# Kernel tuning notes

Hardware: AMD Instinct MI355X
Metric: run time of the kernel (lower is better)

The kernel has to match this reference:

```python
import jax, jax.numpy as jnp
import numpy as np

K, D = 8, 32            # num_heads, out_dim
NA, NP_, DIN = 50000, 100000, 128
SLOPE = 0.2


def _leaky(x):
    return jnp.where(x >= 0, x, SLOPE * x)


def _micro(fs, fd, attn, src, dst, n_dst):
    """GAT-style micro conv for one relation.
    fs: (N_src, K, D) projected src feats; fd: (N_dst, K, D); attn: (K, 2D).
    Returns relu'd aggregation (N_dst, K, D)."""
    al, ar = attn[:, :D], attn[:, D:]
    el = (fs * al).sum(-1)                     # (N_src, K)
    er = (fd * ar).sum(-1)                     # (N_dst, K)
    e = _leaky(el[src] + er[dst])              # (E, K)
    m = jax.ops.segment_max(e, dst, num_segments=n_dst)
    a = jnp.exp(e - m[dst])
    s = jax.ops.segment_sum(a, dst, num_segments=n_dst)
    a = a / s[dst]                             # edge softmax over incoming edges
    msg = fs[src] * a[..., None]               # (E, K, D)
    out = jax.ops.segment_sum(msg, dst, num_segments=n_dst)
    return jax.nn.relu(out)


def setup_inputs() -> dict:
    key = jax.random.key(0)
    ks = jax.random.split(key, 24)
    w = lambda k, sh: (jax.random.normal(k, sh, jnp.float32) * 0.05)
    inp = {
        'feat_author': jax.random.normal(ks[0], (NA, DIN), jnp.float32),
        'feat_paper': jax.random.normal(ks[1], (NP_, DIN), jnp.float32),
        'W_micro_author': w(ks[2], (DIN, K * D)),
        'W_micro_paper': w(ks[3], (DIN, K * D)),
        'attn_micro_author': w(ks[4], (K, 2 * D)),
        'attn_micro_paper': w(ks[5], (K, 2 * D)),
        'W_macro_node_author': w(ks[6], (DIN, K * D)),
        'W_macro_node_paper': w(ks[7], (DIN, K * D)),
        'W_rel_writes': w(ks[8], (K * D, K * D)),
        'W_rel_written_by': w(ks[9], (K * D, K * D)),
        'W_rel_cites': w(ks[10], (K * D, K * D)),
        'attn_macro': w(ks[11], (K, 2 * D)),
        'W_res_author': w(ks[12], (DIN, K * D)),
        'b_res_author': jnp.zeros((K * D,), jnp.float32),
        'W_res_paper': w(ks[13], (DIN, K * D)),
        'b_res_paper': jnp.zeros((K * D,), jnp.float32),
        'res_w_author': jax.random.uniform(ks[14], (1,), jnp.float32),
        'res_w_paper': jax.random.uniform(ks[15], (1,), jnp.float32),
        'writes_src': jax.random.randint(ks[16], (500000,), 0, NA, jnp.int32),
        'writes_dst': jax.random.randint(ks[17], (500000,), 0, NP_, jnp.int32),
        'wb_src': jax.random.randint(ks[18], (500000,), 0, NP_, jnp.int32),
        'wb_dst': jax.random.randint(ks[19], (500000,), 0, NA, jnp.int32),
        'cites_src': jax.random.randint(ks[20], (1000000,), 0, NP_, jnp.int32),
        'cites_dst': jax.random.randint(ks[21], (1000000,), 0, NP_, jnp.int32),
    }
    return inp


def reference(feat_author, feat_paper, W_micro_author, W_micro_paper,
              attn_micro_author, attn_micro_paper, W_macro_node_author,
              W_macro_node_paper, W_rel_writes, W_rel_written_by, W_rel_cites,
              attn_macro, W_res_author, b_res_author, W_res_paper, b_res_paper,
              res_w_author, res_w_paper, writes_src, writes_dst, wb_src, wb_dst,
              cites_src, cites_dst):
    # ---- micro-level (per-relation GAT) ----
    fa = (feat_author @ W_micro_author).reshape(NA, K, D)
    fp = (feat_paper @ W_micro_paper).reshape(NP_, K, D)
    r_writes = _micro(fa, fp, attn_micro_author, writes_src, writes_dst, NP_)   # (NP,K,D)
    r_wb = _micro(fp, fa, attn_micro_paper, wb_src, wb_dst, NA)                 # (NA,K,D)
    r_cites = _micro(fp, fp, attn_micro_paper, cites_src, cites_dst, NP_)       # (NP,K,D)

    # ---- macro-level (cross-relation attention) ----
    rf_writes = (r_writes.reshape(NP_, K * D) @ W_rel_writes).reshape(NP_, K, D)
    rf_wb = (r_wb.reshape(NA, K * D) @ W_rel_written_by).reshape(NA, K, D)
    rf_cites = (r_cites.reshape(NP_, K * D) @ W_rel_cites).reshape(NP_, K, D)

    # author: single incoming relation -> passthrough
    out_a = rf_wb.reshape(NA, K * D)

    # paper: two relations -> stacked attention over relation axis
    node_p = (feat_paper @ W_macro_node_paper).reshape(NP_, K, D)
    stacked = jnp.stack([rf_writes, rf_cites], axis=0)            # (2, NP, K, D)
    cat = jnp.concatenate(
        [jnp.broadcast_to(node_p, stacked.shape), stacked], axis=-1)  # (2, NP, K, 2D)
    scores = _leaky((attn_macro * cat).sum(-1, keepdims=True))    # (2, NP, K, 1)
    wgt = jax.nn.softmax(scores, axis=0)
    out_p = (wgt * stacked).sum(0).reshape(NP_, K * D)

    # ---- residual ----
    aa = jax.nn.sigmoid(res_w_author)
    out_a = aa * out_a + (1 - aa) * (feat_author @ W_res_author + b_res_author)
    ap = jax.nn.sigmoid(res_w_paper)
    out_p = ap * out_p + (1 - ap) * (feat_paper @ W_res_paper + b_res_paper)
    return out_a, out_p
```

## Files before the change

kernel.cpp:

```cpp
#include <hip/hip_runtime.h>
#include <hip/hip_bf16.h>
#include <cstddef>
#include <cstdint>

#define NAU 50000
#define NPA 100000
#define KH 8
#define DH 32
#define KD 256
#define DIN 128
#define SLOPE 0.2f

typedef __attribute__((ext_vector_type(8))) short short8;
typedef __attribute__((ext_vector_type(4))) float f32x4;

__device__ __forceinline__ float leakyf(float x) { return x >= 0.f ? x : SLOPE * x; }

__device__ __forceinline__ ushort f2b(float f) {
  __hip_bfloat16 h = __float2bfloat16(f);
  return *reinterpret_cast<ushort*>(&h);
}
__device__ __forceinline__ float b2f(ushort u) {
  __hip_bfloat16 h;
  *reinterpret_cast<ushort*>(&h) = u;
  return __bfloat162float(h);
}


__device__ __forceinline__ short8 ldfrag(const ushort (*P)[40], int row, int kq) {
  const ushort* p0 = &P[row][kq * 4];
  ushort4 a = *reinterpret_cast<const ushort4*>(p0);
  ushort4 b = *reinterpret_cast<const ushort4*>(p0 + 16);
  short8 f;
  f[0] = (short)a.x; f[1] = (short)a.y; f[2] = (short)a.z; f[3] = (short)a.w;
  f[4] = (short)b.x; f[5] = (short)b.y; f[6] = (short)b.z; f[7] = (short)b.w;
  return f;
}

template<int NP, int EPI>
__global__ __launch_bounds__(256) void k_mfma(
    const float* __restrict__ A0, int K0, const ushort* __restrict__ B0h, const ushort* __restrict__ B0l,
    const float* __restrict__ A1, int K1, const ushort* __restrict__ B1h, const ushort* __restrict__ B1l,
    const float* __restrict__ A2, int K2, const ushort* __restrict__ B2h, const ushort* __restrict__ B2l,
    int M,
    const float* __restrict__ bres, const float* __restrict__ resw,
    const float* __restrict__ wwp, const float* __restrict__ wcp,
    float* __restrict__ outp)
{
  __shared__ ushort As[2][64][40];
  __shared__ ushort Bs[2][64][40];
  const int tid = threadIdx.x;
  const int row0 = blockIdx.x * 64, col0 = blockIdx.y * 64;
  const int wid = tid >> 6, lane = tid & 63;
  const int wr = wid >> 1, wc = wid & 1;
  const int kq = lane >> 4, rr = lane & 15;
  const int sr = tid >> 2;
  const int sc = (tid & 3) << 3;

  f32x4 acc[NP][2][2] = {};

  const float*  Aps[3] = {A0, A1, A2};
  const ushort* Bhs[3] = {B0h, B1h, B2h};
  const ushort* Bls[3] = {B0l, B1l, B2l};
  const int     Kds[3] = {K0, K1, K2};

#pragma unroll
  for (int p = 0; p < NP; ++p) {
    const float*  A  = Aps[p];
    const ushort* Bh = Bhs[p];
    const ushort* Bl = Bls[p];
    const int     Kd = Kds[p];
    for (int k0 = 0; k0 < Kd; k0 += 32) {
      __syncthreads();
      {
        int gr = row0 + sr;
        float4 v0, v1;
        if (gr < M) {
          const float* ap = A + (size_t)gr * Kd + k0 + sc;
          v0 = *reinterpret_cast<const float4*>(ap);
          v1 = *reinterpret_cast<const float4*>(ap + 4);
        } else {
          v0 = make_float4(0.f, 0.f, 0.f, 0.f); v1 = v0;
        }
        float vb[8] = {v0.x, v0.y, v0.z, v0.w, v1.x, v1.y, v1.z, v1.w};
        union Pack { ushort u[8]; int4 v; } ph, pl;
#pragma unroll
        for (int i = 0; i < 8; ++i) {
          ushort h = f2b(vb[i]);
          ph.u[i] = h;
          pl.u[i] = f2b(vb[i] - b2f(h));
        }
        *reinterpret_cast<int4*>(&As[0][sr][sc]) = ph.v;
        *reinterpret_cast<int4*>(&As[1][sr][sc]) = pl.v;
      }
      {
        const size_t bo = (size_t)(col0 + sr) * Kd + k0 + sc;
        *reinterpret_cast<int4*>(&Bs[0][sr][sc]) = *reinterpret_cast<const int4*>(Bh + bo);
        *reinterpret_cast<int4*>(&Bs[1][sr][sc]) = *reinterpret_cast<const int4*>(Bl + bo);
      }
      __syncthreads();

      short8 ah[2], al[2], bh[2], bl[2];
#pragma unroll
      for (int fm = 0; fm < 2; ++fm) {
        int row = wr * 32 + fm * 16 + rr;
        ah[fm] = ldfrag(As[0], row, kq);
        al[fm] = ldfrag(As[1], row, kq);
      }
#pragma unroll
      for (int fn = 0; fn < 2; ++fn) {
        int nrow = wc * 32 + fn * 16 + rr;
        bh[fn] = ldfrag(Bs[0], nrow, kq);
        bl[fn] = ldfrag(Bs[1], nrow, kq);
      }
#pragma unroll
      for (int fm = 0; fm < 2; ++fm)
#pragma unroll
        for (int fn = 0; fn < 2; ++fn) {
          f32x4 c = acc[p][fm][fn];
          c = __builtin_amdgcn_mfma_f32_16x16x32_bf16(ah[fm], bh[fn], c, 0, 0, 0);
          c = __builtin_amdgcn_mfma_f32_16x16x32_bf16(ah[fm], bl[fn], c, 0, 0, 0);
          c = __builtin_amdgcn_mfma_f32_16x16x32_bf16(al[fm], bh[fn], c, 0, 0, 0);
          acc[p][fm][fn] = c;
        }
    }
  }

  float g = 0.f;
  if constexpr (EPI >= 1) g = 1.f / (1.f + __expf(-resw[0]));
#pragma unroll
  for (int fm = 0; fm < 2; ++fm)
#pragma unroll
    for (int fn = 0; fn < 2; ++fn) {
      int cc = col0 + wc * 32 + fn * 16 + rr;
#pragma unroll
      for (int i = 0; i < 4; ++i) {
        int r = row0 + wr * 32 + fm * 16 + kq * 4 + i;
        if (r < M) {
          if constexpr (EPI == 0) {
            outp[(size_t)r * KD + cc] = acc[0][fm][fn][i];
          } else if constexpr (EPI == 1) {
            float o = g * acc[0][fm][fn][i] + (1.f - g) * (acc[1][fm][fn][i] + bres[cc]);
            outp[(size_t)r * KD + cc] = o;
          } else {
            int head = cc >> 5;
            float wwv = wwp[(size_t)r * KH + head];
            float wcv = wcp[(size_t)r * KH + head];
            float o = g * (wwv * acc[0][fm][fn][i] + wcv * acc[1][fm][fn][i])
                    + (1.f - g) * (acc[2][fm][fn][i] + bres[cc]);
            outp[(size_t)r * KD + cc] = o;
          }
        }
      }
    }
}

__global__ void k_prepB(const float* __restrict__ W, int Kd,
                        ushort* __restrict__ Bh, ushort* __restrict__ Bl) {
  int idx = blockIdx.x * 256 + threadIdx.x;
  if (idx >= Kd * 256) return;
  int n = idx / Kd, k = idx - n * Kd;
  float v = W[(size_t)k * 256 + n];
  ushort h = f2b(v);
  Bh[idx] = h;
  Bl[idx] = f2b(v - b2f(h));
}

__global__ void k_node_dots(
    const float* __restrict__ f, int N,
    const float* __restrict__ a0, float* __restrict__ o0,
    const float* __restrict__ a1, float* __restrict__ o1,
    const float* __restrict__ a2, float* __restrict__ o2)
{
  int idx = blockIdx.x * blockDim.x + threadIdx.x;
  if (idx >= N * KH) return;
  int n = idx >> 3, k = idx & 7;
  const float* fr = f + (size_t)n * KD + k * DH;
  float d0 = 0.f, d1 = 0.f, d2 = 0.f;
#pragma unroll
  for (int i = 0; i < DH; i += 4) {
    float4 fv = *reinterpret_cast<const float4*>(fr + i);
    if (a0) {
      float4 v = *reinterpret_cast<const float4*>(a0 + k * 64 + i);
      d0 += fv.x * v.x + fv.y * v.y + fv.z * v.z + fv.w * v.w;
    }
    if (a1) {
      float4 v = *reinterpret_cast<const float4*>(a1 + k * 64 + i);
      d1 += fv.x * v.x + fv.y * v.y + fv.z * v.z + fv.w * v.w;
    }
    if (a2) {
      float4 v = *reinterpret_cast<const float4*>(a2 + k * 64 + i);
      d2 += fv.x * v.x + fv.y * v.y + fv.z * v.z + fv.w * v.w;
    }
  }
  if (o0) o0[idx] = d0;
  if (o1) o1[idx] = d1;
  if (o2) o2[idx] = d2;
}

__global__ void k_hist(const int* __restrict__ dst, int E, int* __restrict__ cnt) {
  int e = blockIdx.x * 256 + threadIdx.x;
  if (e < E) atomicAdd(&cnt[dst[e]], 1);
}

__global__ void k_scan1(const int* __restrict__ cnt, int n,
                        int* __restrict__ off, int* __restrict__ bsum) {
  __shared__ int sm[256];
  int t = threadIdx.x;
  int i = blockIdx.x * 256 + t;
  int v = (i < n) ? cnt[i] : 0;
  sm[t] = v; __syncthreads();
  for (int o = 1; o < 256; o <<= 1) {
    int x = (t >= o) ? sm[t - o] : 0;
    __syncthreads();
    sm[t] += x;
    __syncthreads();
  }
  if (i < n) off[i] = sm[t] - v;
  if (t == 255) bsum[blockIdx.x] = sm[255];
}

__global__ void k_scan2(int* __restrict__ bsum, int nb) {
  __shared__ int sm[512];
  int t = threadIdx.x;
  int v = (t < nb) ? bsum[t] : 0;
  sm[t] = v; __syncthreads();
  for (int o = 1; o < 512; o <<= 1) {
    int x = (t >= o) ? sm[t - o] : 0;
    __syncthreads();
    sm[t] += x;
    __syncthreads();
  }
  if (t < nb) bsum[t] = sm[t] - v;
}

__global__ void k_scan3(int* __restrict__ off, int n, const int* __restrict__ bsum) {
  int i = blockIdx.x * 256 + threadIdx.x;
  if (i < n) off[i] += bsum[blockIdx.x];
}

__global__ void k_scatter(const int* __restrict__ dst, int E,
                          const int* __restrict__ off, int* __restrict__ cur,
                          int* __restrict__ eidx) {
  int e = blockIdx.x * 256 + threadIdx.x;
  if (e >= E) return;
  int d = dst[e];
  int p = atomicAdd(&cur[d], 1);
  eidx[off[d] + p] = e;
}

__global__ __launch_bounds__(256) void k_agg_dst(
    const int* __restrict__ eidx, const int* __restrict__ off_,
    const int* __restrict__ cnt_, const int* __restrict__ src,
    const float* __restrict__ el, const float* __restrict__ er,
    const float* __restrict__ fs, float* __restrict__ outp)
{
  __shared__ int ssi[256];
  int d = blockIdx.x;
  int t = threadIdx.x;
  int k = t >> 5;
  int c = cnt_[d];
  float acc = 0.f;
  float s = 0.f;
  if (c > 0) {
    int base = off_[d];
    float erk = er[(size_t)d * KH + k];
    for (int j0 = 0; j0 < c; j0 += 256) {
      int m = min(256, c - j0);
      __syncthreads();
      if (t < m) ssi[t] = src[eidx[base + j0 + t]];
      __syncthreads();
      for (int j = 0; j < m; ++j) {
        int si = ssi[j];
        float a = __expf(leakyf(el[(size_t)si * KH + k] + erk));
        s += a;
        acc = fmaf(fs[(size_t)si * KD + t], a, acc);
      }
    }
    acc = fmaxf(acc / s, 0.f);
  }
  outp[(size_t)d * KD + t] = acc;
}

__global__ void k_weff(
    const float* __restrict__ Wmnp, const float* __restrict__ Wrw,
    const float* __restrict__ Wrc, const float* __restrict__ attn,
    float* __restrict__ enp, float* __restrict__ ew, float* __restrict__ ec)
{
  int idx = blockIdx.x * blockDim.x + threadIdx.x;
  if (idx < DIN * KH) {
    int c = idx >> 3, k = idx & 7;
    float sum = 0.f;
    for (int d = 0; d < DH; ++d) sum += Wmnp[(size_t)c * KD + k * DH + d] * attn[k * 64 + d];
    enp[idx] = sum;
  } else if (idx < DIN * KH + KD * KH) {
    int j = idx - DIN * KH;
    int c = j >> 3, k = j & 7;
    float sum = 0.f;
    for (int d = 0; d < DH; ++d) sum += Wrw[(size_t)c * KD + k * DH + d] * attn[k * 64 + 32 + d];
    ew[j] = sum;
  } else if (idx < DIN * KH + 2 * KD * KH) {
    int j = idx - DIN * KH - KD * KH;
    int c = j >> 3, k = j & 7;
    float sum = 0.f;
    for (int d = 0; d < DH; ++d) sum += Wrc[(size_t)c * KD + k * DH + d] * attn[k * 64 + 32 + d];
    ec[j] = sum;
  }
}

template<bool RELU>
__global__ __launch_bounds__(256) void k_skinny(
    const float* __restrict__ A, int M, int Kdim,
    const float* __restrict__ W, float* __restrict__ outp)
{
  __shared__ float Ws[KD * KH];
  int tid = threadIdx.x;
  for (int i = tid; i < Kdim * KH; i += 256) Ws[i] = W[i];
  __syncthreads();
  int r = blockIdx.x * 32 + (tid >> 3);
  int k = tid & 7;
  if (r >= M) return;
  const float* Ar = A + (size_t)r * Kdim;
  float acc = 0.f;
  for (int c = 0; c < Kdim; c += 4) {
    float4 av = *reinterpret_cast<const float4*>(Ar + c);
    if (RELU) {
      av.x = fmaxf(av.x, 0.f); av.y = fmaxf(av.y, 0.f);
      av.z = fmaxf(av.z, 0.f); av.w = fmaxf(av.w, 0.f);
    }
    acc += av.x * Ws[(c + 0) * KH + k] + av.y * Ws[(c + 1) * KH + k]
         + av.z * Ws[(c + 2) * KH + k] + av.w * Ws[(c + 3) * KH + k];
  }
  outp[(size_t)r * KH + k] = acc;
}

__global__ void k_weights(
    const float* __restrict__ npdot, const float* __restrict__ scw,
    const float* __restrict__ scc, float* __restrict__ ww,
    float* __restrict__ wc, int N8)
{
  int idx = blockIdx.x * blockDim.x + threadIdx.x;
  if (idx >= N8) return;
  float nd = npdot[idx];
  float lw = leakyf(nd + scw[idx]);
  float lc = leakyf(nd + scc[idx]);
  float m = fmaxf(lw, lc);
  float e1 = __expf(lw - m), e2 = __expf(lc - m);
  float inv = 1.f / (e1 + e2);
  ww[idx] = e1 * inv;
  wc[idx] = e2 * inv;
}

static inline void run_relation(hipStream_t stream,
                                const int* src, const int* dst, int E, int n_dst,
                                int* cnt, int* cur, int* off, int* bsum, int* eidx,
                                const float* el, const float* er,
                                const float* fs, float* outp) {
  hipMemsetAsync(cnt, 0, (size_t)n_dst * sizeof(int), stream);
  hipMemsetAsync(cur, 0, (size_t)n_dst * sizeof(int), stream);
  int nb = (n_dst + 255) / 256;
  k_hist<<<(E + 255) / 256, 256, 0, stream>>>(dst, E, cnt);
  k_scan1<<<nb, 256, 0, stream>>>(cnt, n_dst, off, bsum);
  k_scan2<<<1, 512, 0, stream>>>(bsum, nb);
  k_scan3<<<nb, 256, 0, stream>>>(off, n_dst, bsum);
  k_scatter<<<(E + 255) / 256, 256, 0, stream>>>(dst, E, off, cur, eidx);
  k_agg_dst<<<n_dst, 256, 0, stream>>>(eidx, off, cnt, src, el, er, fs, outp);
}

extern "C" void kernel_launch(void* const* d_in, const int* in_sizes, int n_in,
                              void* d_out, int out_size, void* d_ws, size_t ws_size,
                              hipStream_t stream)
{
  const float* feat_a  = (const float*)d_in[0];
  const float* feat_p  = (const float*)d_in[1];
  const float* W_mic_a = (const float*)d_in[2];
  const float* W_mic_p = (const float*)d_in[3];
  const float* attn_a  = (const float*)d_in[4];
  const float* attn_p  = (const float*)d_in[5];
  const float* W_mnp   = (const float*)d_in[7];
  const float* W_rw    = (const float*)d_in[8];
  const float* W_rwb   = (const float*)d_in[9];
  const float* W_rc    = (const float*)d_in[10];
  const float* attn_m  = (const float*)d_in[11];
  const float* W_res_a = (const float*)d_in[12];
  const float* b_res_a = (const float*)d_in[13];
  const float* W_res_p = (const float*)d_in[14];
  const float* b_res_p = (const float*)d_in[15];
  const float* rw_a    = (const float*)d_in[16];
  const float* rw_p    = (const float*)d_in[17];
  const int* w_src  = (const int*)d_in[18];
  const int* w_dst  = (const int*)d_in[19];
  const int* wbsrc  = (const int*)d_in[20];
  const int* wbdst  = (const int*)d_in[21];
  const int* c_src  = (const int*)d_in[22];
  const int* c_dst  = (const int*)d_in[23];
  const int Ew = in_sizes[18], Ewb = in_sizes[20], Ec = in_sizes[22];

  float* ws = (float*)d_ws;
  const size_t SA = (size_t)NAU * KD;
  const size_t SP = (size_t)NPA * KD;
  float* fa    = ws;
  float* fp    = fa + SA;
  float* r_w   = fp + SP;
  float* r_wb  = r_w + SP;
  float* r_c   = r_wb + SA;
  float* elA   = r_c + SP;
  float* erA   = elA + (size_t)NAU * KH;
  float* elP   = erA + (size_t)NAU * KH;
  float* erPa  = elP + (size_t)NPA * KH;
  float* erPp  = erPa + (size_t)NPA * KH;
  float* npdot = erPp + (size_t)NPA * KH;
  float* scw   = npdot + (size_t)NPA * KH;
  float* scc   = scw + (size_t)NPA * KH;
  float* wwb   = scc + (size_t)NPA * KH;
  float* wcb   = wwb + (size_t)NPA * KH;
  float* effnp = wcb + (size_t)NPA * KH;
  float* effw  = effnp + DIN * KH;
  float* effc  = effw + KD * KH;
  ushort* bt = (ushort*)(effc + KD * KH);
  ushort* BTmicA_h = bt;                  bt += 256 * DIN;
  ushort* BTmicA_l = bt;                  bt += 256 * DIN;
  ushort* BTmicP_h = bt;                  bt += 256 * DIN;
  ushort* BTmicP_l = bt;                  bt += 256 * DIN;
  ushort* BTrwb_h  = bt;                  bt += 256 * KD;
  ushort* BTrwb_l  = bt;                  bt += 256 * KD;
  ushort* BTrw_h   = bt;                  bt += 256 * KD;
  ushort* BTrw_l   = bt;                  bt += 256 * KD;
  ushort* BTrc_h   = bt;                  bt += 256 * KD;
  ushort* BTrc_l   = bt;                  bt += 256 * KD;
  ushort* BTresA_h = bt;                  bt += 256 * DIN;
  ushort* BTresA_l = bt;                  bt += 256 * DIN;
  ushort* BTresP_h = bt;                  bt += 256 * DIN;
  ushort* BTresP_l = bt;                  bt += 256 * DIN;
  int*   cnt   = (int*)bt;
  int*   cur   = cnt + NPA;
  int*   off   = cur + NPA;
  int*   bsum  = off + NPA;
  int*   eidx  = bsum + 512;

  float* out_a = (float*)d_out;
  float* out_p = (float*)d_out + SA;

  k_prepB<<<DIN, 256, 0, stream>>>(W_mic_a, DIN, BTmicA_h, BTmicA_l);
  k_prepB<<<DIN, 256, 0, stream>>>(W_mic_p, DIN, BTmicP_h, BTmicP_l);
  k_prepB<<<KD,  256, 0, stream>>>(W_rwb,  KD,  BTrwb_h,  BTrwb_l);
  k_prepB<<<KD,  256, 0, stream>>>(W_rw,   KD,  BTrw_h,   BTrw_l);
  k_prepB<<<KD,  256, 0, stream>>>(W_rc,   KD,  BTrc_h,   BTrc_l);
  k_prepB<<<DIN, 256, 0, stream>>>(W_res_a, DIN, BTresA_h, BTresA_l);
  k_prepB<<<DIN, 256, 0, stream>>>(W_res_p, DIN, BTresP_h, BTresP_l);

  {
    dim3 g((NAU + 63) / 64, 4);
    k_mfma<1, 0><<<g, 256, 0, stream>>>(
        feat_a, DIN, BTmicA_h, BTmicA_l,
        nullptr, 0, nullptr, nullptr, nullptr, 0, nullptr, nullptr,
        NAU, nullptr, nullptr, nullptr, nullptr, fa);
  }
  {
    dim3 g((NPA + 63) / 64, 4);
    k_mfma<1, 0><<<g, 256, 0, stream>>>(
        feat_p, DIN, BTmicP_h, BTmicP_l,
        nullptr, 0, nullptr, nullptr, nullptr, 0, nullptr, nullptr,
        NPA, nullptr, nullptr, nullptr, nullptr, fp);
  }

  k_node_dots<<<(NAU * KH + 255) / 256, 256, 0, stream>>>(
      fa, NAU, attn_a, elA, attn_p + 32, erA, nullptr, nullptr);
  k_node_dots<<<(NPA * KH + 255) / 256, 256, 0, stream>>>(
      fp, NPA, attn_p, elP, attn_a + 32, erPa, attn_p + 32, erPp);

  run_relation(stream, w_src, w_dst, Ew, NPA, cnt, cur, off, bsum, eidx,
               elA, erPa, fa, r_w);
  run_relation(stream, wbsrc, wbdst, Ewb, NAU, cnt, cur, off, bsum, eidx,
               elP, erA, fp, r_wb);
  run_relation(stream, c_src, c_dst, Ec, NPA, cnt, cur, off, bsum, eidx,
               elP, erPp, fp, r_c);

  {
    dim3 g((NAU + 63) / 64, 4);
    k_mfma<2, 1><<<g, 256, 0, stream>>>(
        r_wb, KD, BTrwb_h, BTrwb_l,
        feat_a, DIN, BTresA_h, BTresA_l,
        nullptr, 0, nullptr, nullptr,
        NAU, b_res_a, rw_a, nullptr, nullptr, out_a);
  }

  k_weff<<<20, 256, 0, stream>>>(W_mnp, W_rw, W_rc, attn_m, effnp, effw, effc);
  k_skinny<false><<<(NPA + 31) / 32, 256, 0, stream>>>(feat_p, NPA, DIN, effnp, npdot);
  k_skinny<true ><<<(NPA + 31) / 32, 256, 0, stream>>>(r_w, NPA, KD, effw, scw);
  k_skinny<true ><<<(NPA + 31) / 32, 256, 0, stream>>>(r_c, NPA, KD, effc, scc);
  k_weights<<<(NPA * KH + 255) / 256, 256, 0, stream>>>(npdot, scw, scc, wwb, wcb, NPA * KH);

  {
    dim3 g((NPA + 63) / 64, 4);
    k_mfma<3, 2><<<g, 256, 0, stream>>>(
        r_w, KD, BTrw_h, BTrw_l,
        r_c, KD, BTrc_h, BTrc_l,
        feat_p, DIN, BTresP_h, BTresP_l,
        NPA, b_res_p, rw_p, wwb, wcb, out_p);
  }
}
```

Before: 1.532 ms.

## Fuse macro score dots into aggregation, swizzle GEMM LDS, remap workgroups, unroll gather

The macro-attention score dot products (r_w·effw, r_c·effc) are now computed in the epilogue of the per-destination aggregation kernel through wave shuffles. This removes two separate skinny passes that re-read the 100k×256 relation outputs. The MFMA GEMM changes its LDS layout to a single 64-wide XOR-swizzled tile holding hi and lo halves, so each fragment is one 16-byte load. It also replaces the bf16 conversion with truncating bit masks and launches a 1D grid with an XCD-aware workgroup remap. The aggregation inner loop is unrolled by four to keep more gathers in flight. Truncating instead of rounding for the hi part changes the split-bf16 precision slightly.

```diff
diff --git a/kernel.cpp b/kernel.cpp
--- a/kernel.cpp
+++ b/kernel.cpp
@@ -27,14 +27,8 @@
 }
 
 
-__device__ __forceinline__ short8 ldfrag(const ushort (*P)[40], int row, int kq) {
-  const ushort* p0 = &P[row][kq * 4];
-  ushort4 a = *reinterpret_cast<const ushort4*>(p0);
-  ushort4 b = *reinterpret_cast<const ushort4*>(p0 + 16);
-  short8 f;
-  f[0] = (short)a.x; f[1] = (short)a.y; f[2] = (short)a.z; f[3] = (short)a.w;
-  f[4] = (short)b.x; f[5] = (short)b.y; f[6] = (short)b.z; f[7] = (short)b.w;
-  return f;
+__device__ __forceinline__ short8 ldfrag8(const ushort (*P)[64], int row, int slot) {
+  return *reinterpret_cast<const short8*>(&P[row][((slot ^ (row & 7)) << 3)]);
 }
 
 template<int NP, int EPI>
@@ -47,15 +41,22 @@
     const float* __restrict__ wwp, const float* __restrict__ wcp,
     float* __restrict__ outp)
 {
-  __shared__ ushort As[2][64][40];
-  __shared__ ushort Bs[2][64][40];
+  __shared__ ushort As[64][64];
+  __shared__ ushort Bs[64][64];
   const int tid = threadIdx.x;
-  const int row0 = blockIdx.x * 64, col0 = blockIdx.y * 64;
+
+  const int nwg = gridDim.x;
+  int orig = blockIdx.x;
+  int q = nwg >> 3, r8 = nwg & 7, xc = orig & 7, jj = orig >> 3;
+  int wg = (xc < r8 ? xc * (q + 1) : r8 * (q + 1) + (xc - r8) * q) + jj;
+  const int row0 = (wg >> 2) * 64, col0 = (wg & 3) * 64;
+
   const int wid = tid >> 6, lane = tid & 63;
   const int wr = wid >> 1, wc = wid & 1;
   const int kq = lane >> 4, rr = lane & 15;
   const int sr = tid >> 2;
-  const int sc = (tid & 3) << 3;
+  const int sq = tid & 3;
+  const int swz = sr & 7;
 
   f32x4 acc[NP][2][2] = {};
 
@@ -74,29 +75,36 @@
       __syncthreads();
       {
         int gr = row0 + sr;
-        float4 v0, v1;
+        float4 v0 = make_float4(0.f, 0.f, 0.f, 0.f), v1 = v0;
         if (gr < M) {
-          const float* ap = A + (size_t)gr * Kd + k0 + sc;
+          const float* ap = A + (size_t)gr * Kd + k0 + sq * 8;
           v0 = *reinterpret_cast<const float4*>(ap);
           v1 = *reinterpret_cast<const float4*>(ap + 4);
-        } else {
-          v0 = make_float4(0.f, 0.f, 0.f, 0.f); v1 = v0;
         }
-        float vb[8] = {v0.x, v0.y, v0.z, v0.w, v1.x, v1.y, v1.z, v1.w};
-        union Pack { ushort u[8]; int4 v; } ph, pl;
-#pragma unroll
-        for (int i = 0; i < 8; ++i) {
-          ushort h = f2b(vb[i]);
-          ph.u[i] = h;
-          pl.u[i] = f2b(vb[i] - b2f(h));
+        float f[8] = {v0.x, v0.y, v0.z, v0.w, v1.x, v1.y, v1.z, v1.w};
+        uint hv[4], lv[4];
+#pragma unroll
+        for (int i = 0; i < 4; ++i) {
+          uint ua = __float_as_uint(f[2 * i]);
+          uint ub = __float_as_uint(f[2 * i + 1]);
+          uint ma = ua & 0xffff0000u;
+          uint mb = ub & 0xffff0000u;
+          hv[i] = (ua >> 16) | mb;
+          float la = f[2 * i] - __uint_as_float(ma);
+          float lb = f[2 * i + 1] - __uint_as_float(mb);
+          lv[i] = (__float_as_uint(la) >> 16) | (__float_as_uint(lb) & 0xffff0000u);
         }
-        *reinterpret_cast<int4*>(&As[0][sr][sc]) = ph.v;
-        *reinterpret_cast<int4*>(&As[1][sr][sc]) = pl.v;
+        *reinterpret_cast<int4*>(&As[sr][((sq ^ swz) << 3)]) =
+            make_int4((int)hv[0], (int)hv[1], (int)hv[2], (int)hv[3]);
+        *reinterpret_cast<int4*>(&As[sr][(((sq + 4) ^ swz) << 3)]) =
+            make_int4((int)lv[0], (int)lv[1], (int)lv[2], (int)lv[3]);
       }
       {
-        const size_t bo = (size_t)(col0 + sr) * Kd + k0 + sc;
-        *reinterpret_cast<int4*>(&Bs[0][sr][sc]) = *reinterpret_cast<const int4*>(Bh + bo);
-        *reinterpret_cast<int4*>(&Bs[1][sr][sc]) = *reinterpret_cast<const int4*>(Bl + bo);
+        const size_t bo = (size_t)(col0 + sr) * Kd + k0 + sq * 8;
+        *reinterpret_cast<int4*>(&Bs[sr][((sq ^ swz) << 3)]) =
+            *reinterpret_cast<const int4*>(Bh + bo);
+        *reinterpret_cast<int4*>(&Bs[sr][(((sq + 4) ^ swz) << 3)]) =
+            *reinterpret_cast<const int4*>(Bl + bo);
       }
       __syncthreads();
 
@@ -104,14 +112,14 @@
 #pragma unroll
       for (int fm = 0; fm < 2; ++fm) {
         int row = wr * 32 + fm * 16 + rr;
-        ah[fm] = ldfrag(As[0], row, kq);
-        al[fm] = ldfrag(As[1], row, kq);
+        ah[fm] = ldfrag8(As, row, kq);
+        al[fm] = ldfrag8(As, row, kq + 4);
       }
 #pragma unroll
       for (int fn = 0; fn < 2; ++fn) {
         int nrow = wc * 32 + fn * 16 + rr;
-        bh[fn] = ldfrag(Bs[0], nrow, kq);
-        bl[fn] = ldfrag(Bs[1], nrow, kq);
+        bh[fn] = ldfrag8(Bs, nrow, kq);
+        bl[fn] = ldfrag8(Bs, nrow, kq + 4);
       }
 #pragma unroll
       for (int fm = 0; fm < 2; ++fm)
@@ -253,15 +261,17 @@
     const int* __restrict__ eidx, const int* __restrict__ off_,
     const int* __restrict__ cnt_, const int* __restrict__ src,
     const float* __restrict__ el, const float* __restrict__ er,
-    const float* __restrict__ fs, float* __restrict__ outp)
+    const float* __restrict__ fs,
+    const float* __restrict__ effv, float* __restrict__ scout,
+    float* __restrict__ outp)
 {
   __shared__ int ssi[256];
+  __shared__ float red[4][8];
   int d = blockIdx.x;
   int t = threadIdx.x;
   int k = t >> 5;
   int c = cnt_[d];
-  float acc = 0.f;
-  float s = 0.f;
+  float acc = 0.f, s = 0.f;
   if (c > 0) {
     int base = off_[d];
     float erk = er[(size_t)d * KH + k];
@@ -270,16 +280,50 @@
       __syncthreads();
       if (t < m) ssi[t] = src[eidx[base + j0 + t]];
       __syncthreads();
-      for (int j = 0; j < m; ++j) {
-        int si = ssi[j];
-        float a = __expf(leakyf(el[(size_t)si * KH + k] + erk));
-        s += a;
-        acc = fmaf(fs[(size_t)si * KD + t], a, acc);
+      for (int j = 0; j < m; j += 4) {
+        int i1 = min(j + 1, m - 1), i2 = min(j + 2, m - 1), i3 = min(j + 3, m - 1);
+        int s0 = ssi[j], s1 = ssi[i1], s2 = ssi[i2], s3 = ssi[i3];
+        float v0 = fs[(size_t)s0 * KD + t];
+        float v1 = fs[(size_t)s1 * KD + t];
+        float v2 = fs[(size_t)s2 * KD + t];
+        float v3 = fs[(size_t)s3 * KD + t];
+        float e0 = el[(size_t)s0 * KH + k];
+        float e1 = el[(size_t)s1 * KH + k];
+        float e2 = el[(size_t)s2 * KH + k];
+        float e3 = el[(size_t)s3 * KH + k];
+        float a0 = __expf(leakyf(e0 + erk));
+        float a1 = (j + 1 < m) ? __expf(leakyf(e1 + erk)) : 0.f;
+        float a2 = (j + 2 < m) ? __expf(leakyf(e2 + erk)) : 0.f;
+        float a3 = (j + 3 < m) ? __expf(leakyf(e3 + erk)) : 0.f;
+        s += (a0 + a1) + (a2 + a3);
+        acc = fmaf(v0, a0, acc);
+        acc = fmaf(v1, a1, acc);
+        acc = fmaf(v2, a2, acc);
+        acc = fmaf(v3, a3, acc);
       }
     }
     acc = fmaxf(acc / s, 0.f);
   }
   outp[(size_t)d * KD + t] = acc;
+  if (effv) {
+    float4 e0 = *reinterpret_cast<const float4*>(effv + t * KH);
+    float4 e1 = *reinterpret_cast<const float4*>(effv + t * KH + 4);
+    float pk[8] = {acc * e0.x, acc * e0.y, acc * e0.z, acc * e0.w,
+                   acc * e1.x, acc * e1.y, acc * e1.z, acc * e1.w};
+#pragma unroll
+    for (int o = 1; o < 64; o <<= 1) {
+#pragma unroll
+      for (int kk = 0; kk < 8; ++kk) pk[kk] += __shfl_xor(pk[kk], o);
+    }
+    int wv = t >> 6, ln = t & 63;
+    if (ln == 0) {
+#pragma unroll
+      for (int kk = 0; kk < 8; ++kk) red[wv][kk] = pk[kk];
+    }
+    __syncthreads();
+    if (t < KH)
+      scout[(size_t)d * KH + t] = (red[0][t] + red[1][t]) + (red[2][t] + red[3][t]);
+  }
 }
 
 __global__ void k_weff(
@@ -355,7 +399,8 @@
                                 const int* src, const int* dst, int E, int n_dst,
                                 int* cnt, int* cur, int* off, int* bsum, int* eidx,
                                 const float* el, const float* er,
-                                const float* fs, float* outp) {
+                                const float* fs, const float* effv, float* scout,
+                                float* outp) {
   hipMemsetAsync(cnt, 0, (size_t)n_dst * sizeof(int), stream);
   hipMemsetAsync(cur, 0, (size_t)n_dst * sizeof(int), stream);
   int nb = (n_dst + 255) / 256;
@@ -364,7 +409,7 @@
   k_scan2<<<1, 512, 0, stream>>>(bsum, nb);
   k_scan3<<<nb, 256, 0, stream>>>(off, n_dst, bsum);
   k_scatter<<<(E + 255) / 256, 256, 0, stream>>>(dst, E, off, cur, eidx);
-  k_agg_dst<<<n_dst, 256, 0, stream>>>(eidx, off, cnt, src, el, er, fs, outp);
+  k_agg_dst<<<n_dst, 256, 0, stream>>>(eidx, off, cnt, src, el, er, fs, effv, scout, outp);
 }
 
 extern "C" void kernel_launch(void* const* d_in, const int* in_sizes, int n_in,
@@ -448,17 +493,18 @@
   k_prepB<<<KD,  256, 0, stream>>>(W_rc,   KD,  BTrc_h,   BTrc_l);
   k_prepB<<<DIN, 256, 0, stream>>>(W_res_a, DIN, BTresA_h, BTresA_l);
   k_prepB<<<DIN, 256, 0, stream>>>(W_res_p, DIN, BTresP_h, BTresP_l);
+  k_weff<<<20, 256, 0, stream>>>(W_mnp, W_rw, W_rc, attn_m, effnp, effw, effc);
 
   {
-    dim3 g((NAU + 63) / 64, 4);
-    k_mfma<1, 0><<<g, 256, 0, stream>>>(
+    int nwg = ((NAU + 63) / 64) * 4;
+    k_mfma<1, 0><<<nwg, 256, 0, stream>>>(
         feat_a, DIN, BTmicA_h, BTmicA_l,
         nullptr, 0, nullptr, nullptr, nullptr, 0, nullptr, nullptr,
         NAU, nullptr, nullptr, nullptr, nullptr, fa);
   }
   {
-    dim3 g((NPA + 63) / 64, 4);
-    k_mfma<1, 0><<<g, 256, 0, stream>>>(
+    int nwg = ((NPA + 63) / 64) * 4;
+    k_mfma<1, 0><<<nwg, 256, 0, stream>>>(
         feat_p, DIN, BTmicP_h, BTmicP_l,
         nullptr, 0, nullptr, nullptr, nullptr, 0, nullptr, nullptr,
         NPA, nullptr, nullptr, nullptr, nullptr, fp);
@@ -470,30 +516,27 @@
       fp, NPA, attn_p, elP, attn_a + 32, erPa, attn_p + 32, erPp);
 
   run_relation(stream, w_src, w_dst, Ew, NPA, cnt, cur, off, bsum, eidx,
-               elA, erPa, fa, r_w);
+               elA, erPa, fa, effw, scw, r_w);
   run_relation(stream, wbsrc, wbdst, Ewb, NAU, cnt, cur, off, bsum, eidx,
-               elP, erA, fp, r_wb);
+               elP, erA, fp, nullptr, nullptr, r_wb);
   run_relation(stream, c_src, c_dst, Ec, NPA, cnt, cur, off, bsum, eidx,
-               elP, erPp, fp, r_c);
+               elP, erPp, fp, effc, scc, r_c);
 
   {
-    dim3 g((NAU + 63) / 64, 4);
-    k_mfma<2, 1><<<g, 256, 0, stream>>>(
+    int nwg = ((NAU + 63) / 64) * 4;
+    k_mfma<2, 1><<<nwg, 256, 0, stream>>>(
         r_wb, KD, BTrwb_h, BTrwb_l,
         feat_a, DIN, BTresA_h, BTresA_l,
         nullptr, 0, nullptr, nullptr,
         NAU, b_res_a, rw_a, nullptr, nullptr, out_a);
   }
 
-  k_weff<<<20, 256, 0, stream>>>(W_mnp, W_rw, W_rc, attn_m, effnp, effw, effc);
   k_skinny<false><<<(NPA + 31) / 32, 256, 0, stream>>>(feat_p, NPA, DIN, effnp, npdot);
-  k_skinny<true ><<<(NPA + 31) / 32, 256, 0, stream>>>(r_w, NPA, KD, effw, scw);
-  k_skinny<true ><<<(NPA + 31) / 32, 256, 0, stream>>>(r_c, NPA, KD, effc, scc);
   k_weights<<<(NPA * KH + 255) / 256, 256, 0, stream>>>(npdot, scw, scc, wwb, wcb, NPA * KH);
 
   {
-    dim3 g((NPA + 63) / 64, 4);
-    k_mfma<3, 2><<<g, 256, 0, stream>>>(
+    int nwg = ((NPA + 63) / 64) * 4;
+    k_mfma<3, 2><<<nwg, 256, 0, stream>>>(
         r_w, KD, BTrw_h, BTrw_l,
         r_c, KD, BTrc_h, BTrc_l,
         feat_p, DIN, BTresP_h, BTresP_l,
```

After: 1.629 ms. 1.06x slower.
